# Optimization experiments

Measured on AMD Instinct MI355X. Metric: run time of the kernel, lower is better.

The kernel has to match this reference:

```python
import jax, jax.numpy as jnp
import numpy as np

GRID = 256
SENSORS = 128
TSTEPS = 1024
ROWS = SENSORS * TSTEPS      # 131072
COLS = GRID * GRID           # 65536
NNZ = 30_000_000
GAIN = 1.0


def setup_inputs() -> dict:
    key = jax.random.key(0)
    k1, k2, k3, k4 = jax.random.split(key, 4)
    field_map = jax.random.normal(k1, (GRID, GRID), dtype=jnp.float32)
    idx_row = jax.random.randint(k2, (NNZ,), 0, ROWS, dtype=jnp.int64)
    idx_col = jax.random.randint(k3, (NNZ,), 0, COLS, dtype=jnp.int64)
    vals = jax.random.normal(k4, (NNZ,), dtype=jnp.float32)
    return {"field_map": field_map, "idx_row": idx_row, "idx_col": idx_col, "vals": vals}


def reference(field_map, idx_row, idx_col, vals):
    # column-major flatten: permute(1,0).reshape(-1) in the torch source
    flat_field = field_map.T.reshape(-1)                      # [COLS]
    # fused gather-multiply-scatter: sensor_response = A @ flat_field
    contrib = vals * jnp.take(flat_field, idx_col)            # [NNZ]
    response = jax.ops.segment_sum(contrib, idx_row, num_segments=ROWS)  # [ROWS]
    return (response * GAIN).reshape(TSTEPS, SENSORS)
```

## Files before the change

### kernel.cpp

```cpp
#include <hip/hip_runtime.h>
#include <hip/hip_fp16.h>

#define GRID_N     256
#define ROWS_TOTAL 131072
#define NNZ        30000000
#define NGROUPS    (NNZ / 4)

#define NRANGES  8
#define BINS     (ROWS_TOTAL / NRANGES)
#define ATHREADS 1024
#define MAXNB2   64

__device__ __forceinline__ int colmap(int c) {
    return ((c & 255) << 8) | (c >> 8);
}

__device__ __forceinline__ unsigned pack_pair(int row, float val) {
    unsigned hb = __half_as_ushort(__float2half(val));
    unsigned f15 = (hb + 1u) >> 1;
    return ((unsigned)row << 15) | f15;
}

__device__ __forceinline__ float unpack_val(unsigned w) {
    return __half2float(__ushort_as_half((unsigned short)((w & 0x7FFFu) << 1)));
}

__global__ __launch_bounds__(1024) void pack_pairs(
    const float* __restrict__ field,
    const int*   __restrict__ idx_row,
    const int*   __restrict__ idx_col,
    const float* __restrict__ vals,
    unsigned*    __restrict__ pairs)
{
    const int stride = gridDim.x * blockDim.x;
    #pragma unroll 2
    for (int i = blockIdx.x * 1024 + threadIdx.x; i < NGROUPS; i += stride) {
        const int4   r = ((const int4*)idx_row)[i];
        const int4   c = ((const int4*)idx_col)[i];
        const float4 v = ((const float4*)vals)[i];
        uint4 o;
        o.x = pack_pair(r.x, v.x * field[colmap(c.x)]);
        o.y = pack_pair(r.y, v.y * field[colmap(c.y)]);
        o.z = pack_pair(r.z, v.z * field[colmap(c.z)]);
        o.w = pack_pair(r.w, v.w * field[colmap(c.w)]);
        ((uint4*)pairs)[i] = o;
    }
}

__global__ __launch_bounds__(ATHREADS) void range_accum(
    const unsigned* __restrict__ pairs,
    float*          __restrict__ copies,
    int nb2)
{
    __shared__ float bins[BINS];
    const int j  = blockIdx.x >> 3;
    const int p  = blockIdx.x & 7;
    const unsigned lo = (unsigned)p << 14;

    for (int t = threadIdx.x; t < BINS; t += ATHREADS) bins[t] = 0.0f;
    __syncthreads();

    const int start = (int)(((long long)j       * NGROUPS) / nb2);
    const int end   = (int)(((long long)(j + 1) * NGROUPS) / nb2);

    #pragma unroll 2
    for (int g = start + threadIdx.x; g < end; g += ATHREADS) {
        const uint4 w = ((const uint4*)pairs)[g];
        unsigned l0 = (w.x >> 15) - lo;
        if (l0 < (unsigned)BINS) atomicAdd(&bins[l0], unpack_val(w.x));
        unsigned l1 = (w.y >> 15) - lo;
        if (l1 < (unsigned)BINS) atomicAdd(&bins[l1], unpack_val(w.y));
        unsigned l2 = (w.z >> 15) - lo;
        if (l2 < (unsigned)BINS) atomicAdd(&bins[l2], unpack_val(w.z));
        unsigned l3 = (w.w >> 15) - lo;
        if (l3 < (unsigned)BINS) atomicAdd(&bins[l3], unpack_val(w.w));
    }
    __syncthreads();

    float* dst = copies + ((size_t)p * nb2 + j) * BINS;
    for (int t = threadIdx.x; t < BINS; t += ATHREADS) dst[t] = bins[t];
}

__global__ __launch_bounds__(256) void reduce_copies(
    const float* __restrict__ copies,
    float*       __restrict__ out,
    int nb2)
{
    const int r   = blockIdx.x * 256 + threadIdx.x;
    const int p   = r >> 14;
    const int bin = r & (BINS - 1);
    const float* base = copies + ((size_t)p * nb2) * BINS + bin;
    float s = 0.0f;
    #pragma unroll 16
    for (int j = 0; j < nb2; ++j)
        s += base[(size_t)j * BINS];
    out[r] = s;
}

__global__ __launch_bounds__(256) void coo_scatter_kernel(
    const float* __restrict__ field,
    const int*   __restrict__ idx_row,
    const int*   __restrict__ idx_col,
    const float* __restrict__ vals,
    float*       __restrict__ out)
{
    const int i = blockIdx.x * 256 + threadIdx.x;
    if (i >= NGROUPS) return;
    const int4   r = ((const int4*)idx_row)[i];
    const int4   c = ((const int4*)idx_col)[i];
    const float4 v = ((const float4*)vals)[i];
    atomicAdd(&out[r.x], v.x * field[colmap(c.x)]);
    atomicAdd(&out[r.y], v.y * field[colmap(c.y)]);
    atomicAdd(&out[r.z], v.z * field[colmap(c.z)]);
    atomicAdd(&out[r.w], v.w * field[colmap(c.w)]);
}

extern "C" void kernel_launch(void* const* d_in, const int* in_sizes, int n_in,
                              void* d_out, int out_size, void* d_ws, size_t ws_size,
                              hipStream_t stream) {
    const float* field   = (const float*)d_in[0];
    const int*   idx_row = (const int*)d_in[1];
    const int*   idx_col = (const int*)d_in[2];
    const float* vals    = (const float*)d_in[3];
    float*       out     = (float*)d_out;

    const size_t pair_bytes = (size_t)NNZ * sizeof(unsigned);
    const size_t copy_slice = (size_t)NRANGES * BINS * sizeof(float);

    if (ws_size >= pair_bytes + 2 * copy_slice) {
        unsigned* pairs  = (unsigned*)d_ws;
        float*    copies = (float*)((char*)d_ws + pair_bytes);

        int nb2 = (int)((ws_size - pair_bytes) / copy_slice);
        if (nb2 > MAXNB2) nb2 = MAXNB2;

        pack_pairs<<<512, 1024, 0, stream>>>(field, idx_row, idx_col, vals, pairs);
        range_accum<<<nb2 * NRANGES, ATHREADS, 0, stream>>>(pairs, copies, nb2);
        reduce_copies<<<ROWS_TOTAL / 256, 256, 0, stream>>>(copies, out, nb2);
    } else {
        hipMemsetAsync(out, 0, (size_t)out_size * sizeof(float), stream);
        coo_scatter_kernel<<<(NGROUPS + 255) / 256, 256, 0, stream>>>(
            field, idx_row, idx_col, vals, out);
    }
}
```

Baseline: 601.6 us.

## Bucket packed pairs by row range during packing to avoid eightfold rereads

The pack kernel now stages each chunk of packed (row, value) words in shared memory. Each wavefront then compacts the words whose top row bits match its range, using ballot and popcount, into a per-wave FIFO and appends them to that range's global bucket. The accumulate kernel then reads only its own bucket instead of scanning all 30M pairs once per row range, which removes the 8x re-read of the packed array. The cost is that bucket capacity (RCAP) is fixed only slightly above the expected per-range count, so skewed row distributions could overflow and silently drop entries. It also adds an extra small launch to zero the counters.

```diff
diff --git a/kernel.cpp b/kernel.cpp
--- a/kernel.cpp
+++ b/kernel.cpp
@@ -1,7 +1,6 @@
 #include <hip/hip_runtime.h>
 #include <hip/hip_fp16.h>
 
-#define GRID_N     256
 #define ROWS_TOTAL 131072
 #define NNZ        30000000
 #define NGROUPS    (NNZ / 4)
@@ -11,6 +10,16 @@
 #define ATHREADS 1024
 #define MAXNB2   64
 
+#define RCAP        3815536
+#define GCNT_STRIDE 16
+
+#define PB_THREADS   512
+#define PB_BLOCKS    1024
+#define CHUNK_GROUPS 1024
+#define CHUNK_WORDS  (CHUNK_GROUPS * 4)
+#define NCHUNKS      ((NGROUPS + CHUNK_GROUPS - 1) / CHUNK_GROUPS)
+#define FCAP         768
+
 __device__ __forceinline__ int colmap(int c) {
     return ((c & 255) << 8) | (c >> 8);
 }
@@ -23,6 +32,149 @@
 
 __device__ __forceinline__ float unpack_val(unsigned w) {
     return __half2float(__ushort_as_half((unsigned short)((w & 0x7FFFu) << 1)));
+}
+
+__global__ __launch_bounds__(PB_THREADS) void pack_bin(
+    const float* __restrict__ field,
+    const int*   __restrict__ idx_row,
+    const int*   __restrict__ idx_col,
+    const float* __restrict__ vals,
+    unsigned*    __restrict__ binned,
+    unsigned*    __restrict__ gcnt)
+{
+    __shared__ __align__(16) unsigned chunk[CHUNK_WORDS];
+    __shared__ __align__(16) unsigned fifo[NRANGES][FCAP];
+
+    const int tid  = threadIdx.x;
+    const int lane = tid & 63;
+    const unsigned wid = (unsigned)(tid >> 6);
+    unsigned* const dst = binned + (size_t)wid * RCAP;
+    const unsigned long long below = (1ull << lane) - 1ull;
+
+    for (int ck = blockIdx.x; ck < NCHUNKS; ck += gridDim.x) {
+        const int gbase = ck * CHUNK_GROUPS;
+
+        #pragma unroll
+        for (int h = 0; h < 2; ++h) {
+            const int gl = (h << 9) + tid;
+            const int gg = gbase + gl;
+            uint4 o = make_uint4(0u, 0u, 0u, 0u);
+            if (gg < NGROUPS) {
+                const int4   r = ((const int4*)idx_row)[gg];
+                const int4   c = ((const int4*)idx_col)[gg];
+                const float4 v = ((const float4*)vals)[gg];
+                o.x = pack_pair(r.x, v.x * field[colmap(c.x)]);
+                o.y = pack_pair(r.y, v.y * field[colmap(c.y)]);
+                o.z = pack_pair(r.z, v.z * field[colmap(c.z)]);
+                o.w = pack_pair(r.w, v.w * field[colmap(c.w)]);
+            }
+            *(uint4*)&chunk[gl << 2] = o;
+        }
+        __syncthreads();
+
+        unsigned cnt = 0;
+        const uint4* chunk4 = (const uint4*)chunk;
+        #pragma unroll 4
+        for (int s = 0; s < CHUNK_WORDS / 256; ++s) {
+            const uint4 q = chunk4[(s << 6) + lane];
+            #define SCAN1(W) {                                                  \
+                const unsigned w_ = (W);                                        \
+                const bool hit_ = ((w_ >> 29) == wid);                          \
+                const unsigned long long m_ = __ballot(hit_);                   \
+                if (hit_) {                                                     \
+                    const unsigned off_ = cnt + (unsigned)__popcll(m_ & below); \
+                    if (off_ < (unsigned)FCAP) fifo[wid][off_] = w_;            \
+                    else {  \
+                        unsigned gs_ = atomicAdd(&gcnt[wid * GCNT_STRIDE], 4u); \
+                        if (gs_ + 4u <= (unsigned)RCAP) {                       \
+                            uint4 sp_ = make_uint4(w_, 0u, 0u, 0u);             \
+                            *(uint4*)(dst + gs_) = sp_;                         \
+                        }                                                       \
+                    }                                                           \
+                }                                                               \
+                cnt += (unsigned)__popcll(m_);                                  \
+            }
+            SCAN1(q.x); SCAN1(q.y); SCAN1(q.z); SCAN1(q.w);
+            #undef SCAN1
+        }
+        if (cnt > (unsigned)FCAP) cnt = (unsigned)FCAP;
+        const unsigned cntR = (cnt + 3u) & ~3u;
+        if (lane < (int)(cntR - cnt)) fifo[wid][cnt + (unsigned)lane] = 0u;
+
+        asm volatile("s_waitcnt lgkmcnt(0)" ::: "memory");
+
+        unsigned gs0 = 0;
+        if (lane == 0) gs0 = atomicAdd(&gcnt[wid * GCNT_STRIDE], cntR);
+        gs0 = __shfl(gs0, 0);
+
+        const unsigned n4 = cntR >> 2;
+        const uint4* f4 = (const uint4*)fifo[wid];
+        for (unsigned t = (unsigned)lane; t < n4; t += 64u) {
+            const unsigned o4 = gs0 + (t << 2);
+            if (o4 + 4u <= (unsigned)RCAP)
+                *(uint4*)(dst + o4) = f4[t];
+        }
+        __syncthreads();
+    }
+}
+
+__global__ __launch_bounds__(ATHREADS) void bin_accum(
+    const unsigned* __restrict__ binned,
+    const unsigned* __restrict__ gcnt,
+    float*          __restrict__ copies,
+    int nb2)
+{
+    __shared__ float bins[BINS];
+    const int j = blockIdx.x >> 3;
+    const int p = blockIdx.x & 7;
+
+    for (int t = threadIdx.x; t < BINS; t += ATHREADS) bins[t] = 0.0f;
+    __syncthreads();
+
+    unsigned n = gcnt[p * GCNT_STRIDE];
+    if (n > (unsigned)RCAP) n = (unsigned)RCAP;
+    const unsigned n4 = n >> 2;
+    const uint4* src = (const uint4*)(binned + (size_t)p * RCAP);
+    const int start = (int)(((long long)j       * (long long)n4) / nb2);
+    const int end   = (int)(((long long)(j + 1) * (long long)n4) / nb2);
+    const unsigned lo = (unsigned)p << 14;
+
+    #pragma unroll 2
+    for (int g = start + threadIdx.x; g < end; g += ATHREADS) {
+        const uint4 w = src[g];
+        unsigned l0 = (w.x >> 15) - lo;
+        if (l0 < (unsigned)BINS) atomicAdd(&bins[l0], unpack_val(w.x));
+        unsigned l1 = (w.y >> 15) - lo;
+        if (l1 < (unsigned)BINS) atomicAdd(&bins[l1], unpack_val(w.y));
+        unsigned l2 = (w.z >> 15) - lo;
+        if (l2 < (unsigned)BINS) atomicAdd(&bins[l2], unpack_val(w.z));
+        unsigned l3 = (w.w >> 15) - lo;
+        if (l3 < (unsigned)BINS) atomicAdd(&bins[l3], unpack_val(w.w));
+    }
+    __syncthreads();
+
+    float* dstc = copies + ((size_t)p * nb2 + j) * BINS;
+    for (int t = threadIdx.x; t < BINS; t += ATHREADS) dstc[t] = bins[t];
+}
+
+__global__ __launch_bounds__(256) void reduce_copies(
+    const float* __restrict__ copies,
+    float*       __restrict__ out,
+    int nb2)
+{
+    const int r   = blockIdx.x * 256 + threadIdx.x;
+    const int p   = r >> 14;
+    const int bin = r & (BINS - 1);
+    const float* base = copies + ((size_t)p * nb2) * BINS + bin;
+    float s = 0.0f;
+    #pragma unroll 16
+    for (int j = 0; j < nb2; ++j)
+        s += base[(size_t)j * BINS];
+    out[r] = s;
+}
+
+__global__ void zero_cnt(unsigned* __restrict__ g) {
+    g[threadIdx.x] = 0u;
 }
 
 __global__ __launch_bounds__(1024) void pack_pairs(
@@ -81,22 +233,6 @@
     for (int t = threadIdx.x; t < BINS; t += ATHREADS) dst[t] = bins[t];
 }
 
-__global__ __launch_bounds__(256) void reduce_copies(
-    const float* __restrict__ copies,
-    float*       __restrict__ out,
-    int nb2)
-{
-    const int r   = blockIdx.x * 256 + threadIdx.x;
-    const int p   = r >> 14;
-    const int bin = r & (BINS - 1);
-    const float* base = copies + ((size_t)p * nb2) * BINS + bin;
-    float s = 0.0f;
-    #pragma unroll 16
-    for (int j = 0; j < nb2; ++j)
-        s += base[(size_t)j * BINS];
-    out[r] = s;
-}
-
 __global__ __launch_bounds__(256) void coo_scatter_kernel(
     const float* __restrict__ field,
     const int*   __restrict__ idx_row,
@@ -124,10 +260,25 @@
     const float* vals    = (const float*)d_in[3];
     float*       out     = (float*)d_out;
 
-    const size_t pair_bytes = (size_t)NNZ * sizeof(unsigned);
-    const size_t copy_slice = (size_t)NRANGES * BINS * sizeof(float);
-
-    if (ws_size >= pair_bytes + 2 * copy_slice) {
+    const size_t binned_bytes = (size_t)NRANGES * RCAP * sizeof(unsigned);
+    const size_t cnt_bytes    = 1024;
+    const size_t pair_bytes   = (size_t)NNZ * sizeof(unsigned);
+    const size_t copy_slice   = (size_t)NRANGES * BINS * sizeof(float);
+
+    if (ws_size >= binned_bytes + cnt_bytes + 2 * copy_slice) {
+        unsigned* binned = (unsigned*)d_ws;
+        unsigned* gcnt   = (unsigned*)((char*)d_ws + binned_bytes);
+        float*    copies = (float*)((char*)d_ws + binned_bytes + cnt_bytes);
+
+        int nb2 = (int)((ws_size - binned_bytes - cnt_bytes) / copy_slice);
+        if (nb2 > MAXNB2) nb2 = MAXNB2;
+
+        zero_cnt<<<1, NRANGES * GCNT_STRIDE, 0, stream>>>(gcnt);
+        pack_bin<<<PB_BLOCKS, PB_THREADS, 0, stream>>>(field, idx_row, idx_col,
+                                                       vals, binned, gcnt);
+        bin_accum<<<nb2 * NRANGES, ATHREADS, 0, stream>>>(binned, gcnt, copies, nb2);
+        reduce_copies<<<ROWS_TOTAL / 256, 256, 0, stream>>>(copies, out, nb2);
+    } else if (ws_size >= pair_bytes + 2 * copy_slice) {
         unsigned* pairs  = (unsigned*)d_ws;
         float*    copies = (float*)((char*)d_ws + pair_bytes);
 
```

Measured after the change: 619.3 us. 2.9% more time.
